# Kernel tuning notes

Measured on AMD Instinct MI355X. Metric: run time of the kernel, lower is better.

Reference implementation:

```python
import jax, jax.numpy as jnp
import numpy as np

B, L, D = 8, 4096, 1024   # batch, max words, sent_dim
S, SENT_LEN = 255, 16     # sentences per sample, words per sentence (255*16=4080)
START_BOUND = 1           # leading zero-pad region, as in the torch module


def setup_inputs() -> dict:
    key = jax.random.key(0)
    k1, k2, k3, k4 = jax.random.split(key, 4)
    words_emb = jax.random.normal(k1, (B, L, D), jnp.float32)
    sents_emb = jax.random.normal(k2, (B, S, D), jnp.float32)
    # nn.Linear(2D, D): weight [D, 2D], bias [D]
    W1_w = jax.random.normal(k3, (D, 2 * D), jnp.float32) / np.sqrt(2 * D)
    W1_b = jax.random.normal(k4, (D,), jnp.float32) * 0.01
    # sentence-index-per-word map; -1 marks the zero-padded regions
    sm = -np.ones((B, L), np.int32)
    idx = np.repeat(np.arange(S, dtype=np.int32), SENT_LEN)  # [S*SENT_LEN]
    sm[:, START_BOUND:START_BOUND + S * SENT_LEN] = idx
    sent_map = jnp.asarray(sm)
    return {"words_emb": words_emb, "sents_emb": sents_emb,
            "W1_w": W1_w, "W1_b": W1_b, "sent_map": sent_map}


def reference(words_emb, sents_emb, W1_w, W1_b, sent_map):
    # Expand sentence embeddings to word positions via gather; zero outside spans.
    valid = sent_map >= 0                                    # [B, L]
    safe_idx = jnp.clip(sent_map, 0)                         # [B, L]
    gathered = jnp.take_along_axis(sents_emb, safe_idx[..., None], axis=1)  # [B, L, D]
    sents_state_flat = jnp.where(valid[..., None], gathered, 0.0)
    # concat word + sentence features, then Linear + ReLU
    x = jnp.concatenate([words_emb, sents_state_flat], axis=-1)  # [B, L, 2D]
    return jax.nn.relu(jnp.einsum('ble,de->bld', x, W1_w) + W1_b)
```

## Files before the change

kernel.cpp:

```cpp
#include <hip/hip_runtime.h>
#include <stdint.h>

constexpr int kB = 8;
constexpr int kL = 4096;
constexpr int kD = 1024;
constexpr int kS = 255;
constexpr int kM = kB * kL;
constexpr int kK = 2 * kD;
constexpr int kN = kD;

typedef __bf16 bf16x8 __attribute__((ext_vector_type(8)));
typedef float  f32x4  __attribute__((ext_vector_type(4)));

constexpr size_t WS_W    = 0;
constexpr size_t WS_ZP   = (size_t)kN * kK * 2;
constexpr size_t WS_NEED = WS_ZP + 4096;

__device__ __forceinline__ uint32_t pk_bf16x2(float a, float b) {
    uint32_t ua = __float_as_uint(a) + 0x8000u;
    uint32_t ub = __float_as_uint(b) + 0x8000u;
    return __builtin_amdgcn_perm(ub, ua, 0x07060302u);
}

__device__ __forceinline__ void async16(const void* g, void* l) {
    __builtin_amdgcn_global_load_lds(
        (const __attribute__((address_space(1))) uint32_t*)g,
        (__attribute__((address_space(3))) uint32_t*)l, 16, 0, 0);
}

#define WAITVM(n)  asm volatile("s_waitcnt vmcnt(" #n ")" ::: "memory")
#define WAITLGKM0  asm volatile("s_waitcnt lgkmcnt(0)" ::: "memory")

__device__ __forceinline__ void blockbar() {
    __builtin_amdgcn_sched_barrier(0);
    __builtin_amdgcn_s_barrier();
    __builtin_amdgcn_sched_barrier(0);
}

__global__ __launch_bounds__(256)
void cvt_w(const float4* __restrict__ W, uint4* __restrict__ WB,
           uint32_t* __restrict__ zp)
{
    if (blockIdx.x == 0) {
        for (int t = threadIdx.x; t < 1024; t += 256) zp[t] = 0u;
    }
    size_t i = (size_t)blockIdx.x * 256 + threadIdx.x;
    float4 a  = W[2 * i];
    float4 b2 = W[2 * i + 1];
    uint4 o;
    o.x = pk_bf16x2(a.x,  a.y);
    o.y = pk_bf16x2(a.z,  a.w);
    o.z = pk_bf16x2(b2.x, b2.y);
    o.w = pk_bf16x2(b2.z, b2.w);
    WB[i] = o;
}

__global__ __launch_bounds__(512, 2)
void wsib_gemm_v3(const float* __restrict__ words,
                  const float* __restrict__ sents,
                  const uint8_t* __restrict__ WB,
                  const float*   __restrict__ bias,
                  const int*     __restrict__ smap,
                  const float*   __restrict__ zpF,
                  float* __restrict__ out)
{
    __shared__ uint8_t lds[4][2][16384];

    const int tid  = threadIdx.x;
    const int w    = tid >> 6;
    const int lane = tid & 63;

    const int lin = blockIdx.y * gridDim.x + blockIdx.x;
    const int swz = (lin & 7) * 64 + (lin >> 3);
    const int nT = swz & 3;
    const int mT = swz >> 2;

    const int wm = (w >> 2) * 128;
    const int wn = (w & 3) * 64;
    const int fr = lane & 15, quad = lane >> 4;

    float bv[4];
    #pragma unroll
    for (int ni = 0; ni < 4; ++ni) bv[ni] = bias[nT * 256 + wn + ni * 16 + fr];

    const int c = tid & 3;
    const int gR0 = mT * 256 + (tid >> 2);
    const int gR1 = gR0 + 128;
    const float* pW0 = words + (size_t)gR0 * kD + c * 8;
    const float* pW1 = words + (size_t)gR1 * kD + c * 8;
    const int bIdx = gR0 >> 12;
    const int s0 = smap[gR0], s1 = smap[gR1];
    const float* pS0 = (s0 >= 0) ? sents + (size_t)(bIdx * kS + s0) * kD + c * 8
                                 : zpF + c * 8;
    const float* pS1 = (s1 >= 0) ? sents + (size_t)(bIdx * kS + s1) * kD + c * 8
                                 : zpF + c * 8;

    const int rB0 = w * 32 + (lane >> 2);
    const uint8_t* pB0 = WB + (size_t)(nT * 256 + rB0) * (kK * 2) + (lane & 3) * 16;
    const uint8_t* pB1 = pB0 + (size_t)16 * (kK * 2);

    const int offA = (wm + fr) * 64 + quad * 16;
    const int offB = (wn + fr) * 64 + quad * 16;

    f32x4 acc[8][4];
    #pragma unroll
    for (int i = 0; i < 8; ++i)
        #pragma unroll
        for (int j = 0; j < 4; ++j) acc[i][j] = (f32x4){0.f, 0.f, 0.f, 0.f};

    auto stageA_load = [&](int t, float4 (&st)[4]) {
        const float* p0 = (t < 32) ? pW0 + t * 32 : pS0 + (t - 32) * 32;
        const float* p1 = (t < 32) ? pW1 + t * 32 : pS1 + (t - 32) * 32;
        st[0] = ((const float4*)p0)[0];
        st[1] = ((const float4*)p0)[1];
        st[2] = ((const float4*)p1)[0];
        st[3] = ((const float4*)p1)[1];
    };
    auto stageA_write = [&](uint8_t* bufA, const float4 (&st)[4]) {
        uint4 o0, o1;
        o0.x = pk_bf16x2(st[0].x, st[0].y);  o0.y = pk_bf16x2(st[0].z, st[0].w);
        o0.z = pk_bf16x2(st[1].x, st[1].y);  o0.w = pk_bf16x2(st[1].z, st[1].w);
        o1.x = pk_bf16x2(st[2].x, st[2].y);  o1.y = pk_bf16x2(st[2].z, st[2].w);
        o1.z = pk_bf16x2(st[3].x, st[3].y);  o1.w = pk_bf16x2(st[3].z, st[3].w);
        *(uint4*)(bufA + tid * 16)        = o0;
        *(uint4*)(bufA + 8192 + tid * 16) = o1;
    };
    auto stageB_dma = [&](uint8_t* bufB, int t) {
        async16(pB0 + t * 64, bufB + w * 2048);
        async16(pB1 + t * 64, bufB + w * 2048 + 1024);
    };

    {
        float4 st[4];
        #pragma unroll
        for (int t = 0; t < 3; ++t) {
            stageA_load(t, st);
            stageA_write((uint8_t*)lds[t][0], st);
            stageB_dma((uint8_t*)lds[t][1], t);
        }
    }
    WAITLGKM0;
    WAITVM(0);
    blockbar();

    bf16x8 af[4], bfA[4], bfB[4];
    #pragma unroll
    for (int mi = 0; mi < 4; ++mi)
        af[mi] = *(const bf16x8*)((uint8_t*)lds[0][0] + offA + mi * 1024);
    #pragma unroll
    for (int ni = 0; ni < 4; ++ni)
        bfA[ni] = *(const bf16x8*)((uint8_t*)lds[0][1] + offB + ni * 1024);

    auto kstep = [&](int t, bf16x8 (&bfc)[4], bf16x8 (&bfn)[4]) {
        const int tS = t + 3;
        uint8_t* bufT  = (uint8_t*)lds[t & 3][0];
        uint8_t* bufNA = (uint8_t*)lds[(t + 1) & 3][0];
        uint8_t* bufNB = (uint8_t*)lds[(t + 1) & 3][1];
        uint8_t* bufSA = (uint8_t*)lds[tS & 3][0];
        uint8_t* bufSB = (uint8_t*)lds[tS & 3][1];

        float4 st[4];
        if (tS < 64) stageA_load(tS, st);
        bf16x8 ag[4];
        #pragma unroll
        for (int mi = 0; mi < 4; ++mi)
            ag[mi] = *(const bf16x8*)(bufT + offA + (mi + 4) * 1024);
        __builtin_amdgcn_s_setprio(1);
        #pragma unroll
        for (int mi = 0; mi < 4; ++mi)
            #pragma unroll
            for (int ni = 0; ni < 4; ++ni)
                acc[mi][ni] = __builtin_amdgcn_mfma_f32_16x16x32_bf16(
                    af[mi], bfc[ni], acc[mi][ni], 0, 0, 0);
        __builtin_amdgcn_s_setprio(0);

        WAITLGKM0;
        if (t < 62) { WAITVM(6); } else { WAITVM(0); }
        blockbar();

        if (t + 1 < 64) {
            #pragma unroll
            for (int ni = 0; ni < 4; ++ni)
                bfn[ni] = *(const bf16x8*)(bufNB + offB + ni * 1024);
            #pragma unroll
            for (int mi = 0; mi < 4; ++mi)
                af[mi] = *(const bf16x8*)(bufNA + offA + mi * 1024);
        }
        if (tS < 64) {
            stageB_dma(bufSB, tS);
            stageA_write(bufSA, st);
        }
        __builtin_amdgcn_s_setprio(1);
        #pragma unroll
        for (int mi = 0; mi < 4; ++mi)
            #pragma unroll
            for (int ni = 0; ni < 4; ++ni)
                acc[mi + 4][ni] = __builtin_amdgcn_mfma_f32_16x16x32_bf16(
                    ag[mi], bfc[ni], acc[mi + 4][ni], 0, 0, 0);
        __builtin_amdgcn_s_setprio(0);
    };

    #pragma unroll 1
    for (int t2 = 0; t2 < 32; ++t2) {
        kstep(2 * t2,     bfA, bfB);
        kstep(2 * t2 + 1, bfB, bfA);
    }

    const int rowBase = mT * 256 + wm + quad * 4;
    const int colBase = nT * 256 + wn + fr;
    #pragma unroll
    for (int mi = 0; mi < 8; ++mi) {
        #pragma unroll
        for (int ni = 0; ni < 4; ++ni) {
            const int col = colBase + ni * 16;
            #pragma unroll
            for (int r = 0; r < 4; ++r) {
                const int row = rowBase + mi * 16 + r;
                out[(size_t)row * kN + col] = fmaxf(acc[mi][ni][r] + bv[ni], 0.f);
            }
        }
    }
}

#define TILE_M 128
#define TILE_N 128
#define TILE_K 32
#define LDS_STRIDE 20
__global__ __launch_bounds__(256)
void wsib_gemm_fb(const float* __restrict__ words, const float* __restrict__ sents,
                  const float* __restrict__ W, const float* __restrict__ bias,
                  const int* __restrict__ smap, float* __restrict__ out)
{
    __shared__ uint32_t Asm[TILE_M * LDS_STRIDE];
    __shared__ uint32_t Bsm[TILE_N * LDS_STRIDE];
    const int tid = threadIdx.x, nT = blockIdx.x, mT = blockIdx.y;
    const int sRow = tid >> 1, half = tid & 1;
    const int mRow = mT * TILE_M + sRow, bIdx = mRow >> 12;
    const float* wsrc = words + (size_t)mRow * kD + half * 16;
    const int sidx = smap[mRow];
    const float* ssrc = (sidx >= 0) ? sents + ((size_t)bIdx * kS + sidx) * kD + half * 16 : nullptr;
    const float* bsrc = W + (size_t)(nT * TILE_N + sRow) * kK + half * 16;
    uint32_t* adst = &Asm[sRow * LDS_STRIDE + half * 8];
    uint32_t* bdst = &Bsm[sRow * LDS_STRIDE + half * 8];
    const int lane = tid & 63, wv = tid >> 6;
    const int wm = (wv & 1) * 64, wn = (wv >> 1) * 64;
    const int fr = lane & 15, quad = lane >> 4;
    f32x4 acc[4][4];
    #pragma unroll
    for (int i = 0; i < 4; ++i)
        #pragma unroll
        for (int j = 0; j < 4; ++j) acc[i][j] = (f32x4){0.f, 0.f, 0.f, 0.f};
    float4 ra[4], rb[4];
    {
        const float4* pa = (const float4*)wsrc; const float4* pb = (const float4*)bsrc;
        #pragma unroll
        for (int i = 0; i < 4; ++i) { ra[i] = pa[i]; rb[i] = pb[i]; }
    }
    for (int k0 = 0; k0 < kK; k0 += TILE_K) {
        uint32_t pa[8], pb[8];
        #pragma unroll
        for (int i = 0; i < 4; ++i) {
            pa[2*i] = pk_bf16x2(ra[i].x, ra[i].y); pa[2*i+1] = pk_bf16x2(ra[i].z, ra[i].w);
            pb[2*i] = pk_bf16x2(rb[i].x, rb[i].y); pb[2*i+1] = pk_bf16x2(rb[i].z, rb[i].w);
        }
        __syncthreads();
        ((uint4*)adst)[0] = make_uint4(pa[0], pa[1], pa[2], pa[3]);
        ((uint4*)adst)[1] = make_uint4(pa[4], pa[5], pa[6], pa[7]);
        ((uint4*)bdst)[0] = make_uint4(pb[0], pb[1], pb[2], pb[3]);
        ((uint4*)bdst)[1] = make_uint4(pb[4], pb[5], pb[6], pb[7]);
        __syncthreads();
        const int k1 = k0 + TILE_K;
        if (k1 < kK) {
            const float* asrc = (k1 < kD) ? (wsrc + k1) : (ssrc ? (ssrc + (k1 - kD)) : nullptr);
            if (asrc) { const float4* p = (const float4*)asrc;
                #pragma unroll
                for (int i = 0; i < 4; ++i) ra[i] = p[i];
            } else {
                #pragma unroll
                for (int i = 0; i < 4; ++i) ra[i] = make_float4(0.f, 0.f, 0.f, 0.f);
            }
            const float4* p = (const float4*)(bsrc + k1);
            #pragma unroll
            for (int i = 0; i < 4; ++i) rb[i] = p[i];
        }
        bf16x8 af[4], bfv[4];
        #pragma unroll
        for (int mi = 0; mi < 4; ++mi)
            af[mi] = *(const bf16x8*)&Asm[(wm + mi * 16 + fr) * LDS_STRIDE + quad * 4];
        #pragma unroll
        for (int ni = 0; ni < 4; ++ni)
            bfv[ni] = *(const bf16x8*)&Bsm[(wn + ni * 16 + fr) * LDS_STRIDE + quad * 4];
        #pragma unroll
        for (int mi = 0; mi < 4; ++mi)
            #pragma unroll
            for (int ni = 0; ni < 4; ++ni)
                acc[mi][ni] = __builtin_amdgcn_mfma_f32_16x16x32_bf16(af[mi], bfv[ni], acc[mi][ni], 0, 0, 0);
    }
    const int rowBase = mT * TILE_M + wm, colBase = nT * TILE_N + wn;
    float bv[4];
    #pragma unroll
    for (int ni = 0; ni < 4; ++ni) bv[ni] = bias[colBase + ni * 16 + fr];
    #pragma unroll
    for (int mi = 0; mi < 4; ++mi)
        #pragma unroll
        for (int ni = 0; ni < 4; ++ni) {
            const int col = colBase + ni * 16 + fr;
            #pragma unroll
            for (int r = 0; r < 4; ++r) {
                const int row = rowBase + mi * 16 + quad * 4 + r;
                out[(size_t)row * kN + col] = fmaxf(acc[mi][ni][r] + bv[ni], 0.f);
            }
        }
}

extern "C" void kernel_launch(void* const* d_in, const int* in_sizes, int n_in,
                              void* d_out, int out_size, void* d_ws, size_t ws_size,
                              hipStream_t stream) {
    const float* words = (const float*)d_in[0];
    const float* sents = (const float*)d_in[1];
    const float* W     = (const float*)d_in[2];
    const float* bias  = (const float*)d_in[3];
    const int*   smap  = (const int*)d_in[4];
    float* out = (float*)d_out;

    if (ws_size >= WS_NEED) {
        uint8_t* ws = (uint8_t*)d_ws;
        uint4* WBv    = (uint4*)(ws + WS_W);
        uint32_t* zp  = (uint32_t*)(ws + WS_ZP);
        cvt_w<<<1024, 256, 0, stream>>>((const float4*)W, WBv, zp);
        dim3 grid(kN / 256, kM / 256);
        wsib_gemm_v3<<<grid, 512, 0, stream>>>(
            words, sents, (const uint8_t*)WBv, bias, smap,
            (const float*)(ws + WS_ZP), out);
    } else {
        dim3 grid(kN / TILE_N, kM / TILE_M);
        wsib_gemm_fb<<<grid, 256, 0, stream>>>(words, sents, W, bias, smap, out);
    }
}
```

Before: 401.4 us.

## Stage fp32 activations into LDS via async DMA and convert at fragment read

The A operand (words/sentence rows) is now copied as raw fp32 straight into LDS with async global-to-LDS loads, the same way the B tiles are, instead of going through registers with bf16 packing before an LDS store. Conversion to bf16 moves to the point where MFMA fragments are read from LDS. The ring drops from four stages to three, with a prefetch distance of two. This removes register staging and VALU packing from the load path, at the cost of twice the LDS footprint per A tile (48KB per stage), twice the LDS read traffic for A, and conversion work repeated by each wave that reads a fragment. The larger LDS use may limit how many blocks can be resident per CU.

Result: faster. 380.1 us (-5.3%).

```diff
diff --git a/kernel.cpp b/kernel.cpp
--- a/kernel.cpp
+++ b/kernel.cpp
@@ -56,15 +56,15 @@
 }
 
 __global__ __launch_bounds__(512, 2)
-void wsib_gemm_v3(const float* __restrict__ words,
-                  const float* __restrict__ sents,
-                  const uint8_t* __restrict__ WB,
-                  const float*   __restrict__ bias,
-                  const int*     __restrict__ smap,
-                  const float*   __restrict__ zpF,
-                  float* __restrict__ out)
+void wsib_gemm_v10(const float* __restrict__ words,
+                   const float* __restrict__ sents,
+                   const uint8_t* __restrict__ WB,
+                   const float*   __restrict__ bias,
+                   const int*     __restrict__ smap,
+                   const uint8_t* __restrict__ zp,
+                   float* __restrict__ out)
 {
-    __shared__ uint8_t lds[4][2][16384];
+    __shared__ uint8_t lds[3][49152];
 
     const int tid  = threadIdx.x;
     const int w    = tid >> 6;
@@ -78,29 +78,52 @@
     const int wm = (w >> 2) * 128;
     const int wn = (w & 3) * 64;
     const int fr = lane & 15, quad = lane >> 4;
+    const int lo16 = lane * 16;
+    const int slabA = (w >> 2) * 8;
+    const int slabB = (w & 3) * 4;
 
     float bv[4];
     #pragma unroll
     for (int ni = 0; ni < 4; ++ni) bv[ni] = bias[nT * 256 + wn + ni * 16 + fr];
 
-    const int c = tid & 3;
-    const int gR0 = mT * 256 + (tid >> 2);
-    const int gR1 = gR0 + 128;
-    const float* pW0 = words + (size_t)gR0 * kD + c * 8;
-    const float* pW1 = words + (size_t)gR1 * kD + c * 8;
-    const int bIdx = gR0 >> 12;
-    const int s0 = smap[gR0], s1 = smap[gR1];
-    const float* pS0 = (s0 >= 0) ? sents + (size_t)(bIdx * kS + s0) * kD + c * 8
-                                 : zpF + c * 8;
-    const float* pS1 = (s1 >= 0) ? sents + (size_t)(bIdx * kS + s1) * kD + c * 8
-                                 : zpF + c * 8;
-
-    const int rB0 = w * 32 + (lane >> 2);
-    const uint8_t* pB0 = WB + (size_t)(nT * 256 + rB0) * (kK * 2) + (lane & 3) * 16;
-    const uint8_t* pB1 = pB0 + (size_t)16 * (kK * 2);
-
-    const int offA = (wm + fr) * 64 + quad * 16;
-    const int offB = (wn + fr) * 64 + quad * 16;
+    const int rloc = ((w >> 1) << 4) + fr;
+    const int kbA  = quad * 32 + (w & 1) * 16;
+    const int bIdx = (mT * 256) >> 12;
+    const uint8_t* aw[4];
+    const uint8_t* as[4];
+    #pragma unroll
+    for (int j = 0; j < 4; ++j) {
+        const int row = mT * 256 + j * 64 + rloc;
+        aw[j] = (const uint8_t*)(words + (size_t)row * kD) + kbA;
+        const int s = smap[row];
+        as[j] = (s >= 0) ? (const uint8_t*)(sents + (size_t)(bIdx * kS + s) * kD) + kbA
+                         : zp + kbA;
+    }
+    const int colb = quad * 16;
+    const int r0 = w * 16 + fr;
+    const uint8_t* pB0 = WB + (size_t)(nT * 256 + r0) * 4096 + colb;
+    const uint8_t* pB1 = WB + (size_t)(nT * 256 + r0 + 128) * 4096 + colb;
+
+    auto stage = [&](int buf, int t) {
+        uint8_t* A  = (uint8_t*)lds[buf];
+        uint8_t* Bb = A + 32768;
+        #pragma unroll
+        for (int j = 0; j < 4; ++j) {
+            const uint8_t* s = (t < 32) ? aw[j] + t * 128 : as[j] + (t - 32) * 128;
+            async16(s, A + j * 8192 + w * 1024);
+        }
+        async16(pB0 + t * 64, Bb + w * 1024);
+        async16(pB1 + t * 64, Bb + 8192 + w * 1024);
+    };
+
+    auto readA = [&](const uint8_t* Ab, int slab) -> bf16x8 {
+        f32x4 flo = *(const f32x4*)(Ab + slab * 2048 + lo16);
+        f32x4 fhi = *(const f32x4*)(Ab + slab * 2048 + 1024 + lo16);
+        bf16x8 r;
+        #pragma unroll
+        for (int i = 0; i < 4; ++i) { r[i] = (__bf16)flo[i]; r[i + 4] = (__bf16)fhi[i]; }
+        return r;
+    };
 
     f32x4 acc[8][4];
     #pragma unroll
@@ -108,63 +131,29 @@
         #pragma unroll
         for (int j = 0; j < 4; ++j) acc[i][j] = (f32x4){0.f, 0.f, 0.f, 0.f};
 
-    auto stageA_load = [&](int t, float4 (&st)[4]) {
-        const float* p0 = (t < 32) ? pW0 + t * 32 : pS0 + (t - 32) * 32;
-        const float* p1 = (t < 32) ? pW1 + t * 32 : pS1 + (t - 32) * 32;
-        st[0] = ((const float4*)p0)[0];
-        st[1] = ((const float4*)p0)[1];
-        st[2] = ((const float4*)p1)[0];
-        st[3] = ((const float4*)p1)[1];
-    };
-    auto stageA_write = [&](uint8_t* bufA, const float4 (&st)[4]) {
-        uint4 o0, o1;
-        o0.x = pk_bf16x2(st[0].x, st[0].y);  o0.y = pk_bf16x2(st[0].z, st[0].w);
-        o0.z = pk_bf16x2(st[1].x, st[1].y);  o0.w = pk_bf16x2(st[1].z, st[1].w);
-        o1.x = pk_bf16x2(st[2].x, st[2].y);  o1.y = pk_bf16x2(st[2].z, st[2].w);
-        o1.z = pk_bf16x2(st[3].x, st[3].y);  o1.w = pk_bf16x2(st[3].z, st[3].w);
-        *(uint4*)(bufA + tid * 16)        = o0;
-        *(uint4*)(bufA + 8192 + tid * 16) = o1;
-    };
-    auto stageB_dma = [&](uint8_t* bufB, int t) {
-        async16(pB0 + t * 64, bufB + w * 2048);
-        async16(pB1 + t * 64, bufB + w * 2048 + 1024);
-    };
-
-    {
-        float4 st[4];
-        #pragma unroll
-        for (int t = 0; t < 3; ++t) {
-            stageA_load(t, st);
-            stageA_write((uint8_t*)lds[t][0], st);
-            stageB_dma((uint8_t*)lds[t][1], t);
-        }
-    }
-    WAITLGKM0;
-    WAITVM(0);
+    stage(0, 0);
+    stage(1, 1);
+    WAITVM(6);
     blockbar();
 
     bf16x8 af[4], bfA[4], bfB[4];
     #pragma unroll
     for (int mi = 0; mi < 4; ++mi)
-        af[mi] = *(const bf16x8*)((uint8_t*)lds[0][0] + offA + mi * 1024);
+        af[mi] = readA((const uint8_t*)lds[0], slabA + mi);
     #pragma unroll
     for (int ni = 0; ni < 4; ++ni)
-        bfA[ni] = *(const bf16x8*)((uint8_t*)lds[0][1] + offB + ni * 1024);
-
-    auto kstep = [&](int t, bf16x8 (&bfc)[4], bf16x8 (&bfn)[4]) {
-        const int tS = t + 3;
-        uint8_t* bufT  = (uint8_t*)lds[t & 3][0];
-        uint8_t* bufNA = (uint8_t*)lds[(t + 1) & 3][0];
-        uint8_t* bufNB = (uint8_t*)lds[(t + 1) & 3][1];
-        uint8_t* bufSA = (uint8_t*)lds[tS & 3][0];
-        uint8_t* bufSB = (uint8_t*)lds[tS & 3][1];
-
-        float4 st[4];
-        if (tS < 64) stageA_load(tS, st);
+        bfA[ni] = *(const bf16x8*)((const uint8_t*)lds[0] + 32768 + (slabB + ni) * 1024 + lo16);
+
+    auto kstep = [&](int t, int bufR, bf16x8 (&bfc)[4], bf16x8 (&bfn)[4]) {
+        const int bufN = (bufR == 2) ? 0 : bufR + 1;
+        const int bufS = (bufN == 2) ? 0 : bufN + 1;
+        const uint8_t* Ab = (const uint8_t*)lds[bufR];
+
+        if (t + 2 < 64) stage(bufS, t + 2);
         bf16x8 ag[4];
         #pragma unroll
         for (int mi = 0; mi < 4; ++mi)
-            ag[mi] = *(const bf16x8*)(bufT + offA + (mi + 4) * 1024);
+            ag[mi] = readA(Ab, slabA + 4 + mi);
         __builtin_amdgcn_s_setprio(1);
         #pragma unroll
         for (int mi = 0; mi < 4; ++mi)
@@ -179,16 +168,14 @@
         blockbar();
 
         if (t + 1 < 64) {
+            const uint8_t* AbN = (const uint8_t*)lds[bufN];
+            const uint8_t* BbN = AbN + 32768;
             #pragma unroll
             for (int ni = 0; ni < 4; ++ni)
-                bfn[ni] = *(const bf16x8*)(bufNB + offB + ni * 1024);
+                bfn[ni] = *(const bf16x8*)(BbN + (slabB + ni) * 1024 + lo16);
             #pragma unroll
             for (int mi = 0; mi < 4; ++mi)
-                af[mi] = *(const bf16x8*)(bufNA + offA + mi * 1024);
-        }
-        if (tS < 64) {
-            stageB_dma(bufSB, tS);
-            stageA_write(bufSA, st);
+                af[mi] = readA(AbN, slabA + mi);
         }
         __builtin_amdgcn_s_setprio(1);
         #pragma unroll
@@ -200,10 +187,13 @@
         __builtin_amdgcn_s_setprio(0);
     };
 
+    int bufR = 0;
     #pragma unroll 1
     for (int t2 = 0; t2 < 32; ++t2) {
-        kstep(2 * t2,     bfA, bfB);
-        kstep(2 * t2 + 1, bfB, bfA);
+        kstep(2 * t2, bufR, bfA, bfB);
+        bufR = (bufR == 2) ? 0 : bufR + 1;
+        kstep(2 * t2 + 1, bufR, bfB, bfA);
+        bufR = (bufR == 2) ? 0 : bufR + 1;
     }
 
     const int rowBase = mT * 256 + wm + quad * 4;
@@ -329,9 +319,9 @@
         uint32_t* zp  = (uint32_t*)(ws + WS_ZP);
         cvt_w<<<1024, 256, 0, stream>>>((const float4*)W, WBv, zp);
         dim3 grid(kN / 256, kM / 256);
-        wsib_gemm_v3<<<grid, 512, 0, stream>>>(
+        wsib_gemm_v10<<<grid, 512, 0, stream>>>(
             words, sents, (const uint8_t*)WBv, bias, smap,
-            (const float*)(ws + WS_ZP), out);
+            (const uint8_t*)(ws + WS_ZP), out);
     } else {
         dim3 grid(kN / TILE_N, kM / TILE_M);
         wsib_gemm_fb<<<grid, 256, 0, stream>>>(words, sents, W, bias, smap, out);
```
